# Performance work log

Hardware: AMD Instinct MI355X
Metric: run time of the kernel (lower is better)

The kernel has to match this reference:

```python
import jax, jax.numpy as jnp
import numpy as np
import math

N_HEAD = 16
D_MODEL = 1024
ATT_DIM = D_MODEL // N_HEAD


def setup_inputs() -> dict:
    key = jax.random.key(0)
    ks = jax.random.split(key, 11)
    B, T, D = 2, 2048, D_MODEL
    s = 1.0 / math.sqrt(D)
    return {
        "q": jax.random.normal(ks[0], (B, T, D), jnp.float32),
        "k": jax.random.normal(ks[1], (B, T, D), jnp.float32),
        "v": jax.random.normal(ks[2], (B, T, D), jnp.float32),
        "Wq": jax.random.normal(ks[3], (D, D), jnp.float32) * s,
        "bq": jnp.zeros((D,), jnp.float32),
        "Wk": jax.random.normal(ks[4], (D, D), jnp.float32) * s,
        "bk": jnp.zeros((D,), jnp.float32),
        "Wv": jax.random.normal(ks[5], (D, D), jnp.float32) * s,
        "bv": jnp.zeros((D,), jnp.float32),
        "Wo": jax.random.normal(ks[6], (D, D), jnp.float32) * s,
        "bo": jnp.zeros((D,), jnp.float32),
    }


def reference(q, k, v, Wq, bq, Wk, bk, Wv, bv, Wo, bo):
    B, T, D = q.shape
    H, hd = N_HEAD, ATT_DIM
    # Linear projections (torch Linear: x @ W.T + b)
    qh = (q @ Wq.T + bq).reshape(B, T, H, hd).transpose(0, 2, 1, 3)  # [B,H,T,hd]
    kh = (k @ Wk.T + bk).reshape(B, T, H, hd).transpose(0, 2, 1, 3)
    vh = (v @ Wv.T + bv).reshape(B, T, H, hd).transpose(0, 2, 1, 3)
    scale = 1.0 / math.sqrt(hd)
    score = jnp.einsum("bhqd,bhkd->bhqk", qh, kh) * scale  # [B,H,T,T]
    attn = jax.nn.softmax(score, axis=-1)
    out = jnp.einsum("bhqk,bhkd->bhqd", attn, vh)  # [B,H,T,hd]
    out = out.transpose(0, 2, 1, 3).reshape(B, T, D)
    return out @ Wo.T + bo
```

## Files before the change

### kernel.cpp

```cpp
#include <hip/hip_runtime.h>


typedef __attribute__((ext_vector_type(8))) short bf16x8;
typedef __attribute__((ext_vector_type(4))) float f32x4;
typedef __attribute__((ext_vector_type(4))) unsigned int u32x4;

#define E22 ((size_t)1 << 22)
#define E20 ((size_t)1 << 20)

__device__ __forceinline__ unsigned short f2bf(float x) {
    unsigned int u = __float_as_uint(x);
    u += 0x7fffu + ((u >> 16) & 1u);
    return (unsigned short)(u >> 16);
}
__device__ __forceinline__ unsigned int pk2bf(float a, float b) {
    return __builtin_amdgcn_perm(__float_as_uint(a), __float_as_uint(b), 0x03020706u);
}
__device__ __forceinline__ void gl16(const void* g, void* l) {
    __builtin_amdgcn_global_load_lds(
        (const __attribute__((address_space(1))) void*)g,
        (__attribute__((address_space(3))) void*)l, 16, 0, 0);
}
__device__ __forceinline__ f32x4 mfma16(bf16x8 a, bf16x8 b, f32x4 c) {
    return __builtin_amdgcn_mfma_f32_16x16x32_bf16(a, b, c, 0, 0, 0);
}

__global__ __launch_bounds__(256)
void split_all(const float* __restrict__ q, const float* __restrict__ k,
               const float* __restrict__ v, const float* __restrict__ wq,
               const float* __restrict__ wk, const float* __restrict__ wv,
               const float* __restrict__ wo, unsigned short* __restrict__ ws)
{
    const size_t t = (size_t)blockIdx.x * 256 + threadIdx.x;
    const size_t e = t * 4;
    const float* src; unsigned short* dst; size_t off;
    if (e < 3 * E22) {
        const unsigned int which = (unsigned int)(e >> 22);
        src = which == 0 ? q : (which == 1 ? k : v);
        off = e & (E22 - 1);
        dst = ws + (size_t)which * E22;
    } else {
        const size_t e2 = e - 3 * E22;
        const unsigned int which = (unsigned int)(e2 >> 20);
        off = e2 & (E20 - 1);
        src = which == 0 ? wq : (which == 1 ? wk : (which == 2 ? wv : wo));
        dst = ws + 3 * E22 + (size_t)which * E20;
    }
    const float4 xv = *(const float4*)(src + off);
    ushort4 h4;
    h4.x = f2bf(xv.x); h4.y = f2bf(xv.y); h4.z = f2bf(xv.z); h4.w = f2bf(xv.w);
    *(ushort4*)(dst + off) = h4;
}

__global__ __launch_bounds__(256)
void gemm_qkv(const unsigned short* __restrict__ Xall,
              const unsigned short* __restrict__ Wcat,
              const float* __restrict__ bq, const float* __restrict__ bk,
              const float* __restrict__ bv, unsigned short* __restrict__ Qhp,
              unsigned short* __restrict__ Khp, unsigned short* __restrict__ Vtp)
{
    __shared__ unsigned short Xs[3 * 4096], Ws[3 * 4096];
    const int tid = threadIdx.x;
    const int w = tid >> 6, ln = tid & 63;
    const int quad = ln >> 4, L = ln & 15;
    const int wy = w >> 1, wx = w & 1;

    const int bid = blockIdx.x;
    const int xcd = bid & 7, j = bid >> 3;
    const int gg = xcd * 12 + (j >> 3);
    const int which = gg >> 5, m_i = gg & 31, n_i = j & 7;
    const int m0 = m_i * 128;

    const unsigned short* X = Xall + (size_t)which * E22;
    const unsigned short* W = Wcat + ((size_t)which * 1024 + n_i * 128) * 1024;
    const float* bp = which == 0 ? bq : (which == 1 ? bk : bv);
    unsigned short* outp = which == 0 ? Qhp : (which == 1 ? Khp : Vtp);
    const float qscale = which == 0 ? 0.18033688011f : 1.0f;

    const int ci0 = ln, ci1 = 64 + ln;
    const int row0 = w * 32 + (ci0 >> 2), row1 = w * 32 + (ci1 >> 2);
    const int gc0 = (ci0 & 3) ^ ((row0 >> 1) & 3);
    const int gc1 = (ci1 & 3) ^ ((row1 >> 1) & 3);
    const int lb0 = w * 2048, lb1 = w * 2048 + 1024;
    const unsigned short* Xbp = X + (size_t)m0 * 1024;
    const size_t gx0 = (size_t)row0 * 1024 + gc0 * 8;
    const size_t gx1 = (size_t)row1 * 1024 + gc1 * 8;

    f32x4 acc[4][4];
#pragma unroll
    for (int i = 0; i < 4; ++i)
#pragma unroll
        for (int jj = 0; jj < 4; ++jj) { f32x4 z = {0.f,0.f,0.f,0.f}; acc[i][jj] = z; }

#define QSTAGE(k0_, bo_)                                                       \
    do {                                                                       \
        gl16(Xbp + gx0 + (k0_), (char*)Xs + (bo_) + lb0);                      \
        gl16(W   + gx0 + (k0_), (char*)Ws + (bo_) + lb0);                      \
        gl16(Xbp + gx1 + (k0_), (char*)Xs + (bo_) + lb1);                      \
        gl16(W   + gx1 + (k0_), (char*)Ws + (bo_) + lb1);                      \
    } while (0)

#define QCOMP(eo_)                                                             \
    do {                                                                       \
        const unsigned short* Xc = Xs + (eo_);                                 \
        const unsigned short* Wc = Ws + (eo_);                                 \
        bf16x8 ah[4], bh[4];                                                   \
        _Pragma("unroll")                                                      \
        for (int mt = 0; mt < 4; ++mt) {                                       \
            const int row = wy * 64 + mt * 16 + L;                             \
            ah[mt] = *(const bf16x8*)(Xc + row * 32 +                          \
                                      ((quad ^ ((row >> 1) & 3)) * 8));        \
        }                                                                      \
        _Pragma("unroll")                                                      \
        for (int nt = 0; nt < 4; ++nt) {                                       \
            const int row = wx * 64 + nt * 16 + L;                             \
            bh[nt] = *(const bf16x8*)(Wc + row * 32 +                          \
                                      ((quad ^ ((row >> 1) & 3)) * 8));        \
        }                                                                      \
        _Pragma("unroll")                                                      \
        for (int mt = 0; mt < 4; ++mt)                                         \
            _Pragma("unroll")                                                  \
            for (int nt = 0; nt < 4; ++nt)                                     \
                acc[mt][nt] = mfma16(ah[mt], bh[nt], acc[mt][nt]);             \
    } while (0)

    QSTAGE(0, 0);
    QSTAGE(32, 8192);

    int cur = 0;
    for (int kt = 0; kt < 31; ++kt) {
        asm volatile("s_waitcnt vmcnt(4)" ::: "memory");
        __builtin_amdgcn_s_barrier();
        asm volatile("" ::: "memory");
        if (kt < 30) {
            int st = cur + 2; if (st >= 3) st -= 3;
            QSTAGE((kt + 2) * 32, st * 8192);
        }
        QCOMP(cur * 4096);
        cur = (cur == 2) ? 0 : cur + 1;
    }
    asm volatile("s_waitcnt vmcnt(0)" ::: "memory");
    __builtin_amdgcn_s_barrier();
    asm volatile("" ::: "memory");
    QCOMP(cur * 4096);
#undef QSTAGE
#undef QCOMP

#pragma unroll
    for (int mt = 0; mt < 4; ++mt)
#pragma unroll
        for (int nt = 0; nt < 4; ++nt) {
            const int gm0 = m0 + wy * 64 + mt * 16 + quad * 4;
            const int bn  = n_i * 128 + wx * 64 + nt * 16 + L;
            const float bvv = bp[bn];
            const int hh = bn >> 6, dd = bn & 63;
            if (which < 2) {
#pragma unroll
                for (int r = 0; r < 4; ++r) {
                    const int gm = gm0 + r;
                    const int bb = gm >> 11, tt = gm & 2047;
                    outp[((size_t)(bb * 16 + hh) * 2048 + tt) * 64 + dd] =
                        f2bf((acc[mt][nt][r] + bvv) * qscale);
                }
            } else {
                const int bb = gm0 >> 11, t0 = gm0 & 2047;
                const int c5 = t0 & 31;
                const int p0 = (t0 & ~31) | (((c5 & 15) >> 2) << 3) | ((c5 >> 4) << 2);
                ushort4 pk;
                pk.x = f2bf(acc[mt][nt][0] + bvv);
                pk.y = f2bf(acc[mt][nt][1] + bvv);
                pk.z = f2bf(acc[mt][nt][2] + bvv);
                pk.w = f2bf(acc[mt][nt][3] + bvv);
                *(ushort4*)(outp + ((size_t)(bb * 16 + hh) * 64 + dd) * 2048 + p0) = pk;
            }
        }
}

__global__ __launch_bounds__(256)
void gemm_out(const unsigned short* __restrict__ X, const unsigned short* __restrict__ W,
              const float* __restrict__ bias, float* __restrict__ outp)
{
    __shared__ unsigned short Xs[3 * 4096], Ws[3 * 2048];
    const int tid = threadIdx.x;
    const int w = tid >> 6, ln = tid & 63;
    const int quad = ln >> 4, L = ln & 15;

    const int bid = blockIdx.x;
    const int xcd = bid & 7, j = bid >> 3;
    const int m0 = (xcd * 4 + (j >> 4)) * 128;
    const int n0 = (j & 15) * 64;

    const int cix0 = ln, cix1 = 64 + ln;
    const int rowx0 = w * 32 + (cix0 >> 2), rowx1 = w * 32 + (cix1 >> 2);
    const int gcx0 = (cix0 & 3) ^ ((rowx0 >> 1) & 3);
    const int gcx1 = (cix1 & 3) ^ ((rowx1 >> 1) & 3);
    const int roww = w * 16 + (ln >> 2);
    const int gcw = (ln & 3) ^ ((roww >> 1) & 3);
    const size_t gxx0 = (size_t)(m0 + rowx0) * 1024 + gcx0 * 8;
    const size_t gxx1 = (size_t)(m0 + rowx1) * 1024 + gcx1 * 8;
    const size_t gww  = (size_t)(n0 + roww) * 1024 + gcw * 8;

    f32x4 acc[2][4];
#pragma unroll
    for (int i = 0; i < 2; ++i)
#pragma unroll
        for (int jj = 0; jj < 4; ++jj) { f32x4 z = {0.f,0.f,0.f,0.f}; acc[i][jj] = z; }

#define OSTAGE(k0_, bf_)                                                       \
    do {                                                                       \
        gl16(X + gxx0 + (k0_), (char*)Xs + (bf_) * 8192 + w * 2048);           \
        gl16(X + gxx1 + (k0_), (char*)Xs + (bf_) * 8192 + w * 2048 + 1024);    \
        gl16(W + gww  + (k0_), (char*)Ws + (bf_) * 4096 + w * 1024);           \
    } while (0)

#define OCOMP(bf_)                                                             \
    do {                                                                       \
        const unsigned short* Xc = Xs + (bf_) * 4096;                          \
        const unsigned short* Wc = Ws + (bf_) * 2048;                          \
        bf16x8 ah[2], bh[4];                                                   \
        _Pragma("unroll")                                                      \
        for (int mt = 0; mt < 2; ++mt) {                                       \
            const int row = w * 32 + mt * 16 + L;                              \
            ah[mt] = *(const bf16x8*)(Xc + row * 32 +                          \
                                      ((quad ^ ((row >> 1) & 3)) * 8));        \
        }                                                                      \
        _Pragma("unroll")                                                      \
        for (int nt = 0; nt < 4; ++nt) {                                       \
            const int row = nt * 16 + L;                                       \
            bh[nt] = *(const bf16x8*)(Wc + row * 32 +                          \
                                      ((quad ^ ((row >> 1) & 3)) * 8));        \
        }                                                                      \
        _Pragma("unroll")                                                      \
        for (int mt = 0; mt < 2; ++mt)                                         \
            _Pragma("unroll")                                                  \
            for (int nt = 0; nt < 4; ++nt)                                     \
                acc[mt][nt] = mfma16(ah[mt], bh[nt], acc[mt][nt]);             \
    } while (0)

    OSTAGE(0, 0);
    OSTAGE(32, 1);

    int cur = 0;
    for (int kt = 0; kt < 31; ++kt) {
        asm volatile("s_waitcnt vmcnt(3)" ::: "memory");
        __builtin_amdgcn_s_barrier();
        asm volatile("" ::: "memory");
        if (kt < 30) {
            int st = cur + 2; if (st >= 3) st -= 3;
            OSTAGE((kt + 2) * 32, st);
        }
        OCOMP(cur);
        cur = (cur == 2) ? 0 : cur + 1;
    }
    asm volatile("s_waitcnt vmcnt(0)" ::: "memory");
    __builtin_amdgcn_s_barrier();
    asm volatile("" ::: "memory");
    OCOMP(cur);
#undef OSTAGE
#undef OCOMP

#pragma unroll
    for (int mt = 0; mt < 2; ++mt)
#pragma unroll
        for (int nt = 0; nt < 4; ++nt) {
            const int gm0 = m0 + w * 32 + mt * 16 + quad * 4;
            const int gn  = n0 + nt * 16 + L;
            const float bvv = bias[gn];
#pragma unroll
            for (int r = 0; r < 4; ++r)
                outp[(size_t)(gm0 + r) * 1024 + gn] = acc[mt][nt][r] + bvv;
        }
}

__global__ __launch_bounds__(256, 2)
void flash(const unsigned short* __restrict__ Qh, const unsigned short* __restrict__ Kh,
           const unsigned short* __restrict__ Vt, unsigned short* __restrict__ A)
{
    __shared__ float Rb[8192];
    __shared__ float Lsc[2 * 4 * 64];
    const int tid = threadIdx.x;
    const int w = tid >> 6, ln = tid & 63;
    const int quad = ln >> 4, L = ln & 15;
    const int wq = w & 1, wk = w >> 1;

    const int bid = blockIdx.x;
    const int xcd = bid & 7, j = bid >> 3;
    const int bh_i = xcd * 4 + (j & 3);
    const int qt = j >> 2;
    const int b = bh_i >> 4, h = bh_i & 15;

    const unsigned short* Qb = Qh + ((size_t)bh_i * 2048 + qt * 128 + wq * 64) * 64;
    const unsigned short* Kp = Kh + ((size_t)bh_i * 2048 + wk * 32 + L) * 64 + quad * 8;
    const unsigned short* Vp = Vt + (size_t)bh_i * 64 * 2048 + (size_t)L * 2048 + wk * 32 + quad * 8;

    bf16x8 bq[4][2];
#pragma unroll
    for (int nt = 0; nt < 4; ++nt)
#pragma unroll
        for (int kc = 0; kc < 2; ++kc)
            bq[nt][kc] = *(const bf16x8*)(Qb + (nt * 16 + L) * 64 + kc * 32 + quad * 8);

    const short one_bf = (short)0x3F80;
    bf16x8 bone = {one_bf, one_bf, one_bf, one_bf, one_bf, one_bf, one_bf, one_bf};

    f32x4 o[4][4];
    f32x4 lacc[4];
#pragma unroll
    for (int mtd = 0; mtd < 4; ++mtd)
#pragma unroll
        for (int nt = 0; nt < 4; ++nt) { f32x4 z = {0.f,0.f,0.f,0.f}; o[mtd][nt] = z; }
#pragma unroll
    for (int nt = 0; nt < 4; ++nt) { f32x4 z = {0.f,0.f,0.f,0.f}; lacc[nt] = z; }

#define KLOAD(kt_, dst_)                                                        \
    do {                                                                        \
        _Pragma("unroll")                                                       \
        for (int mt_ = 0; mt_ < 2; ++mt_)                                       \
            _Pragma("unroll")                                                   \
            for (int kc_ = 0; kc_ < 2; ++kc_)                                   \
                dst_[mt_][kc_] = *(const bf16x8*)(Kp +                          \
                    (size_t)((kt_) * 64 + mt_ * 16) * 64 + kc_ * 32);           \
    } while (0)

#define VLOAD(kt_, dst_)                                                        \
    do {                                                                        \
        _Pragma("unroll")                                                       \
        for (int m_ = 0; m_ < 4; ++m_)                                          \
            dst_[m_] = *(const bf16x8*)(Vp + (size_t)(m_ * 16) * 2048 +         \
                                        (kt_) * 64);                            \
    } while (0)

#define COMP(k_, v_)                                                            \
    do {                                                                        \
        f32x4 s[2][4];                                                          \
        _Pragma("unroll")                                                       \
        for (int mt = 0; mt < 2; ++mt)                                          \
            _Pragma("unroll")                                                   \
            for (int nt = 0; nt < 4; ++nt) {                                    \
                f32x4 z = {0.f, 0.f, 0.f, 0.f};                                 \
                z = mfma16(k_[mt][0], bq[nt][0], z);                            \
                z = mfma16(k_[mt][1], bq[nt][1], z);                            \
                s[mt][nt] = z;                                                  \
            }                                                                   \
        bf16x8 pbx[4];                                                          \
        _Pragma("unroll")                                                       \
        for (int nt = 0; nt < 4; ++nt) {                                        \
            u32x4 pd;                                                           \
            pd.x = pk2bf(__builtin_amdgcn_exp2f(s[0][nt][0]),                   \
                         __builtin_amdgcn_exp2f(s[0][nt][1]));                  \
            pd.y = pk2bf(__builtin_amdgcn_exp2f(s[0][nt][2]),                   \
                         __builtin_amdgcn_exp2f(s[0][nt][3]));                  \
            pd.z = pk2bf(__builtin_amdgcn_exp2f(s[1][nt][0]),                   \
                         __builtin_amdgcn_exp2f(s[1][nt][1]));                  \
            pd.w = pk2bf(__builtin_amdgcn_exp2f(s[1][nt][2]),                   \
                         __builtin_amdgcn_exp2f(s[1][nt][3]));                  \
            pbx[nt] = __builtin_bit_cast(bf16x8, pd);                           \
        }                                                                       \
        _Pragma("unroll")                                                       \
        for (int mtd = 0; mtd < 4; ++mtd)                                       \
            _Pragma("unroll")                                                   \
            for (int nt = 0; nt < 4; ++nt)                                      \
                o[mtd][nt] = mfma16(v_[mtd], pbx[nt], o[mtd][nt]);              \
        _Pragma("unroll")                                                       \
        for (int nt = 0; nt < 4; ++nt)                                          \
            lacc[nt] = mfma16(bone, pbx[nt], lacc[nt]);                         \
    } while (0)

    bf16x8 kA[2][2], kB[2][2], vA[4], vB[4];
    KLOAD(0, kA); VLOAD(0, vA);
    KLOAD(1, kB); VLOAD(1, vB);

#pragma unroll 1
    for (int kt = 0; kt < 30; kt += 2) {
        COMP(kA, vA);
        KLOAD(kt + 2, kA); VLOAD(kt + 2, vA);
        COMP(kB, vB);
        KLOAD(kt + 3, kB); VLOAD(kt + 3, vB);
    }
    COMP(kA, vA);
    COMP(kB, vB);
#undef KLOAD
#undef VLOAD
#undef COMP

    __syncthreads();
    if (wk == 1) {
#pragma unroll
        for (int mtd = 0; mtd < 4; ++mtd)
#pragma unroll
            for (int nt = 0; nt < 4; ++nt)
                *(f32x4*)(Rb + wq * 4096 + (mtd * 4 + nt) * 256 + ln * 4) = o[mtd][nt];
#pragma unroll
        for (int nt = 0; nt < 4; ++nt)
            Lsc[wq * 256 + nt * 64 + ln] = lacc[nt][0];
    }
    __syncthreads();
    if (wk == 0) {
#pragma unroll
        for (int mtd = 0; mtd < 4; ++mtd)
#pragma unroll
            for (int nt = 0; nt < 4; ++nt)
                o[mtd][nt] += *(const f32x4*)(Rb + wq * 4096 + (mtd * 4 + nt) * 256 + ln * 4);

#pragma unroll
        for (int nt = 0; nt < 4; ++nt) {
            const float lsum = lacc[nt][0] + Lsc[wq * 256 + nt * 64 + ln];
            const float inv = 1.0f / lsum;
            const int qrow = b * 2048 + qt * 128 + wq * 64 + nt * 16 + L;
#pragma unroll
            for (int mtd = 0; mtd < 4; ++mtd) {
                const int d0 = mtd * 16 + quad * 4;
                ushort4 pk;
                pk.x = f2bf(o[mtd][nt][0] * inv);
                pk.y = f2bf(o[mtd][nt][1] * inv);
                pk.z = f2bf(o[mtd][nt][2] * inv);
                pk.w = f2bf(o[mtd][nt][3] * inv);
                *(ushort4*)(A + (size_t)qrow * 1024 + h * 64 + d0) = pk;
            }
        }
    }
}

extern "C" void kernel_launch(void* const* d_in, const int* in_sizes, int n_in,
                              void* d_out, int out_size, void* d_ws, size_t ws_size,
                              hipStream_t stream) {
    const float* q  = (const float*)d_in[0];
    const float* k  = (const float*)d_in[1];
    const float* v  = (const float*)d_in[2];
    const float* Wq = (const float*)d_in[3];
    const float* bq = (const float*)d_in[4];
    const float* Wk = (const float*)d_in[5];
    const float* bk = (const float*)d_in[6];
    const float* Wv = (const float*)d_in[7];
    const float* bv = (const float*)d_in[8];
    const float* Wo = (const float*)d_in[9];
    const float* bo = (const float*)d_in[10];

    unsigned short* W = (unsigned short*)d_ws;
    unsigned short *Xall = W;
    unsigned short *Wcat = W + 3 * E22;
    unsigned short *Wob  = Wcat + 3 * E20;
    unsigned short *Qhp  = W + 4 * E22;
    unsigned short *Khp  = W + 5 * E22;
    unsigned short *Vtp  = W + 6 * E22;
    unsigned short *A    = W;

    split_all<<<16384, 256, 0, stream>>>(q, k, v, Wq, Wk, Wv, Wo, W);

    gemm_qkv<<<768, 256, 0, stream>>>(Xall, Wcat, bq, bk, bv, Qhp, Khp, Vtp);

    flash<<<512, 256, 0, stream>>>(Qhp, Khp, Vtp, A);

    gemm_out<<<512, 256, 0, stream>>>(A, Wob, bo, (float*)d_out);
}
```

Measured before the change: 237.3 us.

## Stage K/V tiles through swizzled LDS with async global-to-LDS loads

Replaces the per-wave direct global register loads of K and V in the flash kernel with cooperative global_load_lds copies into XOR-swizzled, double-buffered shared memory. Each block loads each K/V tile once instead of both query-half waves fetching the same data. The swizzle is meant to avoid bank conflicts. This adds a block-wide barrier per pair of tiles and raises LDS use to 64KB, which may limit occupancy at launch_bounds(256,2). There is also no explicit wait on the async loads beyond __syncthreads.

```diff
diff --git a/kernel.cpp b/kernel.cpp
--- a/kernel.cpp
+++ b/kernel.cpp
@@ -276,7 +276,7 @@
 void flash(const unsigned short* __restrict__ Qh, const unsigned short* __restrict__ Kh,
            const unsigned short* __restrict__ Vt, unsigned short* __restrict__ A)
 {
-    __shared__ float Rb[8192];
+    __shared__ unsigned short SM[32768];
     __shared__ float Lsc[2 * 4 * 64];
     const int tid = threadIdx.x;
     const int w = tid >> 6, ln = tid & 63;
@@ -290,8 +290,8 @@
     const int b = bh_i >> 4, h = bh_i & 15;
 
     const unsigned short* Qb = Qh + ((size_t)bh_i * 2048 + qt * 128 + wq * 64) * 64;
-    const unsigned short* Kp = Kh + ((size_t)bh_i * 2048 + wk * 32 + L) * 64 + quad * 8;
-    const unsigned short* Vp = Vt + (size_t)bh_i * 64 * 2048 + (size_t)L * 2048 + wk * 32 + quad * 8;
+    const unsigned short* Kb = Kh + (size_t)bh_i * 2048 * 64;
+    const unsigned short* Vb = Vt + (size_t)bh_i * 64 * 2048;
 
     bf16x8 bq[4][2];
 #pragma unroll
@@ -312,34 +312,43 @@
 #pragma unroll
     for (int nt = 0; nt < 4; ++nt) { f32x4 z = {0.f,0.f,0.f,0.f}; lacc[nt] = z; }
 
-#define KLOAD(kt_, dst_)                                                        \
+    const int ci0 = (w * 2 + 0) * 64 + ln, ci1 = (w * 2 + 1) * 64 + ln;
+    const int rr0 = ci0 >> 3, rr1 = ci1 >> 3;
+    const int gc0 = (ci0 & 7) ^ (rr0 & 7), gc1 = (ci1 & 7) ^ (rr1 & 7);
+
+#define STAGE1(kt_, b_, s_)                                                     \
     do {                                                                        \
-        _Pragma("unroll")                                                       \
-        for (int mt_ = 0; mt_ < 2; ++mt_)                                       \
+        gl16(Kb + (size_t)((kt_) * 64 + rr0) * 64 + gc0 * 8,                    \
+             (char*)SM + (b_) * 16384 + (s_) * 8192 + (w * 2 + 0) * 1024);      \
+        gl16(Kb + (size_t)((kt_) * 64 + rr1) * 64 + gc1 * 8,                    \
+             (char*)SM + (b_) * 16384 + (s_) * 8192 + (w * 2 + 1) * 1024);      \
+        gl16(Vb + (size_t)rr0 * 2048 + (kt_) * 64 + gc0 * 8,                    \
+             (char*)SM + 32768 + (b_) * 16384 + (s_) * 8192 + (w * 2 + 0) * 1024); \
+        gl16(Vb + (size_t)rr1 * 2048 + (kt_) * 64 + gc1 * 8,                    \
+             (char*)SM + 32768 + (b_) * 16384 + (s_) * 8192 + (w * 2 + 1) * 1024); \
+    } while (0)
+
+#define SUBCOMP(b_, s_)                                                         \
+    do {                                                                        \
+        const unsigned short* Ksb = SM + (b_) * 8192 + (s_) * 4096;             \
+        const unsigned short* Vsb = SM + 16384 + (b_) * 8192 + (s_) * 4096;     \
+        bf16x8 ak[2][2];                                                        \
+        _Pragma("unroll")                                                       \
+        for (int mt = 0; mt < 2; ++mt)                                          \
             _Pragma("unroll")                                                   \
-            for (int kc_ = 0; kc_ < 2; ++kc_)                                   \
-                dst_[mt_][kc_] = *(const bf16x8*)(Kp +                          \
-                    (size_t)((kt_) * 64 + mt_ * 16) * 64 + kc_ * 32);           \
-    } while (0)
-
-#define VLOAD(kt_, dst_)                                                        \
-    do {                                                                        \
-        _Pragma("unroll")                                                       \
-        for (int m_ = 0; m_ < 4; ++m_)                                          \
-            dst_[m_] = *(const bf16x8*)(Vp + (size_t)(m_ * 16) * 2048 +         \
-                                        (kt_) * 64);                            \
-    } while (0)
-
-#define COMP(k_, v_)                                                            \
-    do {                                                                        \
+            for (int kc = 0; kc < 2; ++kc) {                                    \
+                const int row = wk * 32 + mt * 16 + L;                          \
+                ak[mt][kc] = *(const bf16x8*)(Ksb + row * 64 +                  \
+                                              (((kc * 4 + quad) ^ (L & 7)) * 8)); \
+            }                                                                   \
         f32x4 s[2][4];                                                          \
         _Pragma("unroll")                                                       \
         for (int mt = 0; mt < 2; ++mt)                                          \
             _Pragma("unroll")                                                   \
             for (int nt = 0; nt < 4; ++nt) {                                    \
                 f32x4 z = {0.f, 0.f, 0.f, 0.f};                                 \
-                z = mfma16(k_[mt][0], bq[nt][0], z);                            \
-                z = mfma16(k_[mt][1], bq[nt][1], z);                            \
+                z = mfma16(ak[mt][0], bq[nt][0], z);                            \
+                z = mfma16(ak[mt][1], bq[nt][1], z);                            \
                 s[mt][nt] = z;                                                  \
             }                                                                   \
         bf16x8 pbx[4];                                                          \
@@ -356,34 +365,41 @@
                          __builtin_amdgcn_exp2f(s[1][nt][3]));                  \
             pbx[nt] = __builtin_bit_cast(bf16x8, pd);                           \
         }                                                                       \
+        bf16x8 av[4];                                                           \
+        _Pragma("unroll")                                                       \
+        for (int mtd = 0; mtd < 4; ++mtd) {                                     \
+            const int row = mtd * 16 + L;                                       \
+            av[mtd] = *(const bf16x8*)(Vsb + row * 64 +                         \
+                                       (((wk * 4 + quad) ^ (L & 7)) * 8));      \
+        }                                                                       \
         _Pragma("unroll")                                                       \
         for (int mtd = 0; mtd < 4; ++mtd)                                       \
             _Pragma("unroll")                                                   \
             for (int nt = 0; nt < 4; ++nt)                                      \
-                o[mtd][nt] = mfma16(v_[mtd], pbx[nt], o[mtd][nt]);              \
+                o[mtd][nt] = mfma16(av[mtd], pbx[nt], o[mtd][nt]);              \
         _Pragma("unroll")                                                       \
         for (int nt = 0; nt < 4; ++nt)                                          \
             lacc[nt] = mfma16(bone, pbx[nt], lacc[nt]);                         \
     } while (0)
 
-    bf16x8 kA[2][2], kB[2][2], vA[4], vB[4];
-    KLOAD(0, kA); VLOAD(0, vA);
-    KLOAD(1, kB); VLOAD(1, vB);
-
-#pragma unroll 1
-    for (int kt = 0; kt < 30; kt += 2) {
-        COMP(kA, vA);
-        KLOAD(kt + 2, kA); VLOAD(kt + 2, vA);
-        COMP(kB, vB);
-        KLOAD(kt + 3, kB); VLOAD(kt + 3, vB);
-    }
-    COMP(kA, vA);
-    COMP(kB, vB);
-#undef KLOAD
-#undef VLOAD
-#undef COMP
+    STAGE1(0, 0, 0);
+    STAGE1(1, 0, 1);
+
+    for (int p = 0; p < 16; ++p) {
+        const int cur = p & 1;
+        __syncthreads();
+        if (p < 15) {
+            STAGE1(2 * p + 2, cur ^ 1, 0);
+            STAGE1(2 * p + 3, cur ^ 1, 1);
+        }
+        SUBCOMP(cur, 0);
+        SUBCOMP(cur, 1);
+    }
+#undef STAGE1
+#undef SUBCOMP
 
     __syncthreads();
+    float* Rb = (float*)SM;
     if (wk == 1) {
 #pragma unroll
         for (int mtd = 0; mtd < 4; ++mtd)
```

Result: faster. 211.5 us (-10.9%).
